# Kernel tuning notes

Hardware: AMD Instinct MI355X
Metric: run time of the kernel (lower is better)

## Reference

```python
import jax, jax.numpy as jnp
import numpy as np

B, S, D_IN, D_ST = 4, 4096, 1024, 1024


def setup_inputs() -> dict:
    key = jax.random.key(0)
    ks = jax.random.split(key, 7)
    s_in = 1.0 / np.sqrt(D_IN)
    s_st = 1.0 / np.sqrt(D_ST)
    return {
        "x": jax.random.normal(ks[0], (B, S, D_IN), dtype=jnp.float32),
        "gate_w": jax.random.uniform(ks[1], (D_IN, D_ST), jnp.float32, -s_in, s_in),
        "gate_b": jax.random.uniform(ks[2], (D_ST,), jnp.float32, -s_in, s_in),
        "inp_w": jax.random.uniform(ks[3], (D_IN, D_ST), jnp.float32, -s_in, s_in),
        "inp_b": jax.random.uniform(ks[4], (D_ST,), jnp.float32, -s_in, s_in),
        "out_w": jax.random.uniform(ks[5], (D_ST, D_IN), jnp.float32, -s_st, s_st),
        "out_b": jax.random.uniform(ks[6], (D_IN,), jnp.float32, -s_st, s_st),
    }


def reference(x, gate_w, gate_b, inp_w, inp_b, out_w, out_b):
    # x: [B, S, D_in]
    inp = jnp.einsum("bsd,de->bse", x, inp_w) + inp_b      # [B,S,Dst]
    gate = jax.nn.sigmoid(jnp.einsum("bsd,de->bse", x, gate_w) + gate_b)
    b_t = (1.0 - gate) * inp                               # [B,S,Dst]

    # affine recurrence h_t = gate_t * h_{t-1} + b_t via lax.scan over time
    def step(h, ab):
        a, b = ab
        h = a * h + b
        return h, h

    a_sb = jnp.swapaxes(gate, 0, 1)  # [S,B,Dst]
    b_sb = jnp.swapaxes(b_t, 0, 1)
    h0 = jnp.zeros((x.shape[0], inp.shape[-1]), dtype=x.dtype)
    _, hs = jax.lax.scan(step, h0, (a_sb, b_sb))           # [S,B,Dst]
    scan_out = jnp.swapaxes(hs, 0, 1)                      # [B,S,Dst]

    return x + jnp.einsum("bse,ed->bsd", scan_out, out_w) + out_b
```

## Files before the change

kernel.cpp:

```cpp
#include <hip/hip_runtime.h>

typedef unsigned short u16;
typedef unsigned int   u32;
typedef __bf16 bf16x8 __attribute__((ext_vector_type(8)));
typedef float  f32x4  __attribute__((ext_vector_type(4)));

#define DEVI __device__ __forceinline__

DEVI u16 f2bf(float f) {
    union { float f; u32 u; } c; c.f = f;
    u32 u = c.u;
    u32 r = (u + 0x7fffu + ((u >> 16) & 1u)) >> 16;
    return (u16)r;
}
DEVI float bf2f(u16 v) {
    union { u32 u; float f; } c; c.u = ((u32)v) << 16;
    return c.f;
}

DEVI void gload16(const void* g, void* l) {
    __builtin_amdgcn_global_load_lds(
        (const __attribute__((address_space(1))) void*)g,
        (__attribute__((address_space(3))) void*)l, 16, 0, 0);
}


#define VMW(N)  asm volatile("s_waitcnt vmcnt(" #N ")" ::: "memory")
#define BAR     __builtin_amdgcn_s_barrier()
#define SP1     __builtin_amdgcn_s_setprio(1)
#define SP0     __builtin_amdgcn_s_setprio(0)
#define SCB     __builtin_amdgcn_sched_barrier(0)
#define LGKM0   asm volatile("s_waitcnt lgkmcnt(0)" ::: "memory")
#define LGKM8   asm volatile("s_waitcnt lgkmcnt(8)" ::: "memory")

DEVI void stage_kh(const u16* g, u16* slot, int tid) {
    const int wvb = (tid >> 6) << 9;
    const int r = tid >> 2;
    const int p = tid & 3;
    const int c = p ^ (r & 3);
    const long off = (long)r * 1024 + (c << 3);
    gload16(g + off, slot + wvb);
    gload16(g + off + (long)128 * 1024, slot + 4096 + wvb);
}

DEVI f32x4 mfma(const bf16x8& a, const bf16x8& b, const f32x4& c) {
    return __builtin_amdgcn_mfma_f32_16x16x32_bf16(a, b, c, 0, 0, 0);
}

#define PHASE(I, Q, STAGE_CODE, GATE_CODE)                                   \
    {                                                                        \
        if (I == 0) {                                                        \
            _Pragma("unroll")                                                \
            for (int nf = 0; nf < 4; ++nf) {                                 \
                bh[nf][0] = *(const bf16x8*)(lds + (Q) + 16384 + nf * 512 + bbase); \
                bh[nf][1] = *(const bf16x8*)(lds + (Q) + 24576 + nf * 512 + bbase); \
            }                                                                \
        }                                                                    \
        a00 = *(const bf16x8*)(lds + (Q) + (I) * 1024 + abase);              \
        a01 = *(const bf16x8*)(lds + (Q) + 8192 + (I) * 1024 + abase);       \
        a10 = *(const bf16x8*)(lds + (Q) + (I) * 1024 + 512 + abase);        \
        a11 = *(const bf16x8*)(lds + (Q) + 8192 + (I) * 1024 + 512 + abase); \
        if (I == 0) { LGKM8; }                                               \
        STAGE_CODE;                                                          \
        SCB; BAR;                                                            \
        LGKM0; SCB;                                                          \
        SP1;                                                                 \
        _Pragma("unroll")                                                    \
        for (int nf = 0; nf < 4; ++nf) {                                     \
            acc[(I) * 2][nf]     = mfma(a00, bh[nf][0], acc[(I) * 2][nf]);   \
            acc[(I) * 2][nf]     = mfma(a01, bh[nf][1], acc[(I) * 2][nf]);   \
            acc[(I) * 2 + 1][nf] = mfma(a10, bh[nf][0], acc[(I) * 2 + 1][nf]); \
            acc[(I) * 2 + 1][nf] = mfma(a11, bh[nf][1], acc[(I) * 2 + 1][nf]); \
        }                                                                    \
        SP0;                                                                 \
        GATE_CODE;                                                           \
        BAR;                                                                 \
    }

#define NOSTAGE do {} while (0)
#define NOGATE  do {} while (0)

DEVI void pipe256(const u16* Ab, const u16* Bb, u16* lds,
                  f32x4 (&acc)[8][4], int tid) {
    const int lane = tid & 63;
    const int wm = (tid >> 6) >> 2, wn = (tid >> 6) & 3;
    const int pch = ((lane >> 4) ^ (lane & 3)) << 3;
    const int abase = (wm * 128 + (lane & 15)) * 32 + pch;
    const int bbase = (wn * 64 + (lane & 15)) * 32 + pch;

    stage_kh(Bb,      lds + 16384, tid);
    stage_kh(Bb + 32, lds + 24576, tid);
    stage_kh(Ab,      lds + 0,     tid);
    stage_kh(Ab + 32, lds + 8192,  tid);
    stage_kh(Bb + 64, lds + 49152, tid);
    stage_kh(Bb + 96, lds + 57344, tid);
    VMW(4); BAR;

    bf16x8 bh[4][2];
    bf16x8 a00, a01, a10, a11;

#pragma unroll 1
    for (int j = 0; j < 7; ++j) {
        const u16* A1g = Ab + (2 * j + 1) * 64;
        const u16* A2g = Ab + (2 * j + 2) * 64;
        const u16* B2g = Bb + (2 * j + 2) * 64;
        const u16* B3g = Bb + (2 * j + 3) * 64;
        PHASE(0, 0,
              { stage_kh(A1g, lds + 32768, tid); stage_kh(A1g + 32, lds + 40960, tid); },
              NOGATE);
        PHASE(1, 0,
              { stage_kh(B2g, lds + 16384, tid); stage_kh(B2g + 32, lds + 24576, tid); },
              NOGATE);
        PHASE(2, 0, NOSTAGE, NOGATE);
        PHASE(3, 0, NOSTAGE, VMW(4));
        PHASE(0, 32768,
              { stage_kh(A2g, lds + 0, tid); stage_kh(A2g + 32, lds + 8192, tid); },
              NOGATE);
        PHASE(1, 32768,
              { stage_kh(B3g, lds + 49152, tid); stage_kh(B3g + 32, lds + 57344, tid); },
              NOGATE);
        PHASE(2, 32768, NOSTAGE, NOGATE);
        PHASE(3, 32768, NOSTAGE, VMW(4));
    }
    {
        const u16* A15 = Ab + 15 * 64;
        PHASE(0, 0,
              { stage_kh(A15, lds + 32768, tid); stage_kh(A15 + 32, lds + 40960, tid); },
              NOGATE);
        PHASE(1, 0, NOSTAGE, NOGATE);
        PHASE(2, 0, NOSTAGE, NOGATE);
        PHASE(3, 0, NOSTAGE, VMW(0));
        PHASE(0, 32768, NOSTAGE, NOGATE);
        PHASE(1, 32768, NOSTAGE, NOGATE);
        PHASE(2, 32768, NOSTAGE, NOGATE);
        PHASE(3, 32768, NOSTAGE, NOGATE);
    }
}


__global__ __launch_bounds__(512, 1) void k_gemm_cat8(
    const u16* __restrict__ A, const u16* __restrict__ Bcat,
    const float* __restrict__ gb, const float* __restrict__ ib,
    u32* __restrict__ ab) {
    __shared__ __align__(16) u16 lds[65536];
    const int tid = threadIdx.x, lane = tid & 63;
    const int wm = (tid >> 6) >> 2, wn = (tid >> 6) & 3;

    int fid = (int)blockIdx.y * 8 + (int)blockIdx.x;
    int swz = (fid & 7) * 64 + (fid >> 3);
    const long bn = swz & 7, bm = swz >> 3;

    f32x4 acc[8][4] = {};
    pipe256(A + bm * 256 * 1024, Bcat + bn * 256 * 1024, lds, acc, tid);

    const long rbase = bm * 256 + wm * 128;
    const int chbase = (int)bn * 128 + wn * 32;
#pragma unroll
    for (int t = 0; t < 2; ++t) {
        int ch = chbase + t * 16 + (lane & 15);
        float g0 = gb[ch], i0 = ib[ch];
#pragma unroll
        for (int m = 0; m < 8; ++m) {
            long row = rbase + m * 16 + ((lane >> 4) << 2);
#pragma unroll
            for (int i = 0; i < 4; ++i) {
                float pg = acc[m][2 * t][i] + g0;
                float pi = acc[m][2 * t + 1][i] + i0;
                float aa = 1.0f / (1.0f + __expf(-pg));
                float bb = (1.0f - aa) * pi;
                ab[(row + i) * 1024 + ch] = (u32)f2bf(aa) | ((u32)f2bf(bb) << 16);
            }
        }
    }
}


__global__ __launch_bounds__(512, 1) void k_gemm_out8(
    const u16* __restrict__ A, const u16* __restrict__ Bt,
    const float* __restrict__ xres, const float* __restrict__ ob,
    float* __restrict__ out) {
    __shared__ __align__(16) u16 lds[65536];
    const int tid = threadIdx.x, lane = tid & 63;
    const int wm = (tid >> 6) >> 2, wn = (tid >> 6) & 3;

    int fid = (int)blockIdx.y * 4 + (int)blockIdx.x;
    int swz = (fid & 7) * 32 + (fid >> 3);
    const long bn = swz & 3, bm = swz >> 2;

    f32x4 acc[8][4] = {};
    pipe256(A + bm * 256 * 1024, Bt + bn * 256 * 1024, lds, acc, tid);

    const long rbase = bm * 256 + wm * 128;
    const int cbase = (int)bn * 256 + wn * 64;
#pragma unroll
    for (int n = 0; n < 4; ++n) {
        int col = cbase + n * 16 + (lane & 15);
        float o0 = ob[col];
#pragma unroll
        for (int m = 0; m < 8; ++m) {
            long row = rbase + m * 16 + ((lane >> 4) << 2);
#pragma unroll
            for (int i = 0; i < 4; ++i) {
                long o = (row + i) * 1024 + col;
                out[o] = acc[m][n][i] + o0 + xres[o];
            }
        }
    }
}


__global__ __launch_bounds__(256) void k_cvt_x(const float4* __restrict__ x,
                                               uint2* __restrict__ o, int n4) {
    int i = blockIdx.x * 256 + threadIdx.x;
    if (i < n4) {
        float4 v = x[i];
        uint2 r;
        r.x = (u32)f2bf(v.x) | ((u32)f2bf(v.y) << 16);
        r.y = (u32)f2bf(v.z) | ((u32)f2bf(v.w) << 16);
        o[i] = r;
    }
}

__global__ __launch_bounds__(256) void k_transpose_bf(const float* __restrict__ w,
                                                      u16* __restrict__ wt, int R, int C) {
    __shared__ float t[32][33];
    int c0 = blockIdx.x * 32, r0 = blockIdx.y * 32;
    int x = threadIdx.x & 31, y = threadIdx.x >> 5;
    for (int i = y; i < 32; i += 8) t[i][x] = w[(size_t)(r0 + i) * C + c0 + x];
    __syncthreads();
    for (int i = y; i < 32; i += 8) wt[(size_t)(c0 + i) * R + r0 + x] = f2bf(t[x][i]);
}

__global__ __launch_bounds__(256) void k_transpose_cat(const float* __restrict__ gw,
                                                       const float* __restrict__ iw,
                                                       u16* __restrict__ wt, int K, int C) {
    __shared__ float t[32][33];
    int c0 = blockIdx.x * 32, r0 = blockIdx.y * 32;
    const float* w = blockIdx.z ? iw : gw;
    int x = threadIdx.x & 31, y = threadIdx.x >> 5;
    for (int i = y; i < 32; i += 8) t[i][x] = w[(size_t)(r0 + i) * C + c0 + x];
    __syncthreads();
    for (int i = y; i < 32; i += 8) {
        int ch = c0 + i;
        int r = ((ch >> 4) << 5) | ((int)blockIdx.z << 4) | (ch & 15);
        wt[(size_t)r * K + r0 + x] = f2bf(t[x][i]);
    }
}


__global__ __launch_bounds__(256) void k_scanA(const u32* __restrict__ ab,
                                               float2* __restrict__ cAB) {
    int e = blockIdx.x * 256 + threadIdx.x;
    int c = blockIdx.y, bt = blockIdx.z;
    long base = ((long)bt * 4096 + c * 64) * 1024 + e;
    float Aa = 1.f, H = 0.f;
#pragma unroll 4
    for (int i = 0; i < 64; ++i) {
        u32 v = ab[base + (long)i * 1024];
        float a = bf2f((u16)v), b = bf2f((u16)(v >> 16));
        H = a * H + b;
        Aa *= a;
    }
    cAB[((long)bt * 64 + c) * 1024 + e] = make_float2(Aa, H);
}

__global__ __launch_bounds__(256) void k_scanB(const float2* __restrict__ cAB,
                                               float* __restrict__ hin) {
    int e = blockIdx.x * 256 + threadIdx.x;
    int bt = blockIdx.y;
    float H = 0.f;
#pragma unroll
    for (int c = 0; c < 64; ++c) {
        long s = ((long)bt * 64 + c) * 1024 + e;
        hin[s] = H;
        float2 v = cAB[s];
        H = v.x * H + v.y;
    }
}

__global__ __launch_bounds__(256) void k_scanC(const u32* __restrict__ ab,
                                               const float* __restrict__ hin,
                                               u16* __restrict__ hout) {
    int e = blockIdx.x * 256 + threadIdx.x;
    int c = blockIdx.y, bt = blockIdx.z;
    long base = ((long)bt * 4096 + c * 64) * 1024 + e;
    float H = hin[((long)bt * 64 + c) * 1024 + e];
#pragma unroll 4
    for (int i = 0; i < 64; ++i) {
        u32 v = ab[base + (long)i * 1024];
        H = bf2f((u16)v) * H + bf2f((u16)(v >> 16));
        hout[base + (long)i * 1024] = f2bf(H);
    }
}


extern "C" void kernel_launch(void* const* d_in, const int* in_sizes, int n_in,
                              void* d_out, int out_size, void* d_ws, size_t ws_size,
                              hipStream_t stream) {
    const float* x      = (const float*)d_in[0];
    const float* gate_w = (const float*)d_in[1];
    const float* gate_b = (const float*)d_in[2];
    const float* inp_w  = (const float*)d_in[3];
    const float* inp_b  = (const float*)d_in[4];
    const float* out_w  = (const float*)d_in[5];
    const float* out_b  = (const float*)d_in[6];
    float* out = (float*)d_out;

    const int Bsz = 4, S = 4096, Din = 1024, Dst = 1024;
    const int M = Bsz * S;
    const long nx = (long)M * Din;

    char* w = (char*)d_ws;
    u16* xb      = (u16*)(w);
    u16* catW    = (u16*)(w + 33554432);
    u16* owT     = (u16*)(w + 37748736);
    u16* hbf     = (u16*)(w + 39845888);
    float2* cAB  = (float2*)(w + 73400320);
    float* hin   = (float*)(w + 75497472);

    u32* ab = (u32*)d_out;

    k_cvt_x<<<(int)(nx / 4 / 256), 256, 0, stream>>>((const float4*)x, (uint2*)xb, (int)(nx / 4));
    k_transpose_cat<<<dim3(Dst / 32, Din / 32, 2), 256, 0, stream>>>(gate_w, inp_w, catW, Din, Dst);
    k_transpose_bf<<<dim3(Din / 32, Dst / 32), 256, 0, stream>>>(out_w, owT, Dst, Din);

    k_gemm_cat8<<<dim3(8, M / 256), 512, 0, stream>>>(xb, catW, gate_b, inp_b, ab);

    k_scanA<<<dim3(4, 64, Bsz), 256, 0, stream>>>(ab, cAB);
    k_scanB<<<dim3(4, Bsz), 256, 0, stream>>>(cAB, hin);
    k_scanC<<<dim3(4, 64, Bsz), 256, 0, stream>>>(ab, hin, hbf);

    k_gemm_out8<<<dim3(4, M / 256), 512, 0, stream>>>(hbf, owT, x, out_b, out);
}
```

Before: 187.5 us.

## Replace 64-K phased pipeline with triple-buffered 32-K tiles for two blocks per CU

The GEMM main loop moves from a double-buffered 64-wide K stage, with explicit lgkmcnt waits and sched barriers, to a rotating triple buffer of 32-wide K tiles with one barrier per tile. This shrinks LDS from 128KB to 96KB per block, and launch bounds change to allow two 512-thread blocks per CU, aiming for more occupancy and latency hiding. The risks are the added register pressure from the tighter launch bound, possible spills with an 8x4 accumulator array, and twice as many barriers per unit of K work.

```diff
diff --git a/kernel.cpp b/kernel.cpp
--- a/kernel.cpp
+++ b/kernel.cpp
@@ -29,9 +29,6 @@
 #define BAR     __builtin_amdgcn_s_barrier()
 #define SP1     __builtin_amdgcn_s_setprio(1)
 #define SP0     __builtin_amdgcn_s_setprio(0)
-#define SCB     __builtin_amdgcn_sched_barrier(0)
-#define LGKM0   asm volatile("s_waitcnt lgkmcnt(0)" ::: "memory")
-#define LGKM8   asm volatile("s_waitcnt lgkmcnt(8)" ::: "memory")
 
 DEVI void stage_kh(const u16* g, u16* slot, int tid) {
     const int wvb = (tid >> 6) << 9;
@@ -47,38 +44,48 @@
     return __builtin_amdgcn_mfma_f32_16x16x32_bf16(a, b, c, 0, 0, 0);
 }
 
-#define PHASE(I, Q, STAGE_CODE, GATE_CODE)                                   \
+#define TILE_COMPUTE(q0)                                                     \
     {                                                                        \
-        if (I == 0) {                                                        \
-            _Pragma("unroll")                                                \
-            for (int nf = 0; nf < 4; ++nf) {                                 \
-                bh[nf][0] = *(const bf16x8*)(lds + (Q) + 16384 + nf * 512 + bbase); \
-                bh[nf][1] = *(const bf16x8*)(lds + (Q) + 24576 + nf * 512 + bbase); \
-            }                                                                \
-        }                                                                    \
-        a00 = *(const bf16x8*)(lds + (Q) + (I) * 1024 + abase);              \
-        a01 = *(const bf16x8*)(lds + (Q) + 8192 + (I) * 1024 + abase);       \
-        a10 = *(const bf16x8*)(lds + (Q) + (I) * 1024 + 512 + abase);        \
-        a11 = *(const bf16x8*)(lds + (Q) + 8192 + (I) * 1024 + 512 + abase); \
-        if (I == 0) { LGKM8; }                                               \
-        STAGE_CODE;                                                          \
-        SCB; BAR;                                                            \
-        LGKM0; SCB;                                                          \
+        _Pragma("unroll")                                                    \
+        for (int nf = 0; nf < 4; ++nf)                                       \
+            bh[nf] = *(const bf16x8*)(lds + (q0) + bbase + nf * 512);        \
+        aC0 = *(const bf16x8*)(lds + (q0) + abase);                          \
+        aC1 = *(const bf16x8*)(lds + (q0) + abase + 512);                    \
+        aN0 = *(const bf16x8*)(lds + (q0) + abase + 1024);                   \
+        aN1 = *(const bf16x8*)(lds + (q0) + abase + 1536);                   \
         SP1;                                                                 \
         _Pragma("unroll")                                                    \
         for (int nf = 0; nf < 4; ++nf) {                                     \
-            acc[(I) * 2][nf]     = mfma(a00, bh[nf][0], acc[(I) * 2][nf]);   \
-            acc[(I) * 2][nf]     = mfma(a01, bh[nf][1], acc[(I) * 2][nf]);   \
-            acc[(I) * 2 + 1][nf] = mfma(a10, bh[nf][0], acc[(I) * 2 + 1][nf]); \
-            acc[(I) * 2 + 1][nf] = mfma(a11, bh[nf][1], acc[(I) * 2 + 1][nf]); \
+            acc[0][nf] = mfma(aC0, bh[nf], acc[0][nf]);                      \
+            acc[1][nf] = mfma(aC1, bh[nf], acc[1][nf]);                      \
         }                                                                    \
         SP0;                                                                 \
-        GATE_CODE;                                                           \
-        BAR;                                                                 \
-    }
-
-#define NOSTAGE do {} while (0)
-#define NOGATE  do {} while (0)
+        aC0 = *(const bf16x8*)(lds + (q0) + abase + 2048);                   \
+        aC1 = *(const bf16x8*)(lds + (q0) + abase + 2560);                   \
+        SP1;                                                                 \
+        _Pragma("unroll")                                                    \
+        for (int nf = 0; nf < 4; ++nf) {                                     \
+            acc[2][nf] = mfma(aN0, bh[nf], acc[2][nf]);                      \
+            acc[3][nf] = mfma(aN1, bh[nf], acc[3][nf]);                      \
+        }                                                                    \
+        SP0;                                                                 \
+        aN0 = *(const bf16x8*)(lds + (q0) + abase + 3072);                   \
+        aN1 = *(const bf16x8*)(lds + (q0) + abase + 3584);                   \
+        SP1;                                                                 \
+        _Pragma("unroll")                                                    \
+        for (int nf = 0; nf < 4; ++nf) {                                     \
+            acc[4][nf] = mfma(aC0, bh[nf], acc[4][nf]);                      \
+            acc[5][nf] = mfma(aC1, bh[nf], acc[5][nf]);                      \
+        }                                                                    \
+        SP0;                                                                 \
+        SP1;                                                                 \
+        _Pragma("unroll")                                                    \
+        for (int nf = 0; nf < 4; ++nf) {                                     \
+            acc[6][nf] = mfma(aN0, bh[nf], acc[6][nf]);                      \
+            acc[7][nf] = mfma(aN1, bh[nf], acc[7][nf]);                      \
+        }                                                                    \
+        SP0;                                                                 \
+    }
 
 DEVI void pipe256(const u16* Ab, const u16* Bb, u16* lds,
                   f32x4 (&acc)[8][4], int tid) {
@@ -86,63 +93,36 @@
     const int wm = (tid >> 6) >> 2, wn = (tid >> 6) & 3;
     const int pch = ((lane >> 4) ^ (lane & 3)) << 3;
     const int abase = (wm * 128 + (lane & 15)) * 32 + pch;
-    const int bbase = (wn * 64 + (lane & 15)) * 32 + pch;
-
-    stage_kh(Bb,      lds + 16384, tid);
+    const int bbase = 8192 + (wn * 64 + (lane & 15)) * 32 + pch;
+
+    stage_kh(Ab,      lds + 0,     tid);
+    stage_kh(Bb,      lds + 8192,  tid);
+    stage_kh(Ab + 32, lds + 16384, tid);
     stage_kh(Bb + 32, lds + 24576, tid);
-    stage_kh(Ab,      lds + 0,     tid);
-    stage_kh(Ab + 32, lds + 8192,  tid);
-    stage_kh(Bb + 64, lds + 49152, tid);
-    stage_kh(Bb + 96, lds + 57344, tid);
     VMW(4); BAR;
 
-    bf16x8 bh[4][2];
-    bf16x8 a00, a01, a10, a11;
+    bf16x8 bh[4], aC0, aC1, aN0, aN1;
+    int q0 = 0, q1 = 16384, q2 = 32768;
 
 #pragma unroll 1
-    for (int j = 0; j < 7; ++j) {
-        const u16* A1g = Ab + (2 * j + 1) * 64;
-        const u16* A2g = Ab + (2 * j + 2) * 64;
-        const u16* B2g = Bb + (2 * j + 2) * 64;
-        const u16* B3g = Bb + (2 * j + 3) * 64;
-        PHASE(0, 0,
-              { stage_kh(A1g, lds + 32768, tid); stage_kh(A1g + 32, lds + 40960, tid); },
-              NOGATE);
-        PHASE(1, 0,
-              { stage_kh(B2g, lds + 16384, tid); stage_kh(B2g + 32, lds + 24576, tid); },
-              NOGATE);
-        PHASE(2, 0, NOSTAGE, NOGATE);
-        PHASE(3, 0, NOSTAGE, VMW(4));
-        PHASE(0, 32768,
-              { stage_kh(A2g, lds + 0, tid); stage_kh(A2g + 32, lds + 8192, tid); },
-              NOGATE);
-        PHASE(1, 32768,
-              { stage_kh(B3g, lds + 49152, tid); stage_kh(B3g + 32, lds + 57344, tid); },
-              NOGATE);
-        PHASE(2, 32768, NOSTAGE, NOGATE);
-        PHASE(3, 32768, NOSTAGE, VMW(4));
-    }
-    {
-        const u16* A15 = Ab + 15 * 64;
-        PHASE(0, 0,
-              { stage_kh(A15, lds + 32768, tid); stage_kh(A15 + 32, lds + 40960, tid); },
-              NOGATE);
-        PHASE(1, 0, NOSTAGE, NOGATE);
-        PHASE(2, 0, NOSTAGE, NOGATE);
-        PHASE(3, 0, NOSTAGE, VMW(0));
-        PHASE(0, 32768, NOSTAGE, NOGATE);
-        PHASE(1, 32768, NOSTAGE, NOGATE);
-        PHASE(2, 32768, NOSTAGE, NOGATE);
-        PHASE(3, 32768, NOSTAGE, NOGATE);
-    }
-}
-
-
-__global__ __launch_bounds__(512, 1) void k_gemm_cat8(
+    for (int t = 0; t < 30; ++t) {
+        stage_kh(Ab + (t + 2) * 32, lds + q2, tid);
+        stage_kh(Bb + (t + 2) * 32, lds + q2 + 8192, tid);
+        TILE_COMPUTE(q0);
+        VMW(4); BAR;
+        int tq = q0; q0 = q1; q1 = q2; q2 = tq;
+    }
+    TILE_COMPUTE(q0);
+    VMW(0); BAR;
+    TILE_COMPUTE(q1);
+}
+
+
+__global__ __launch_bounds__(512, 2) void k_gemm_cat8(
     const u16* __restrict__ A, const u16* __restrict__ Bcat,
     const float* __restrict__ gb, const float* __restrict__ ib,
     u32* __restrict__ ab) {
-    __shared__ __align__(16) u16 lds[65536];
+    __shared__ __align__(16) u16 lds[49152];
     const int tid = threadIdx.x, lane = tid & 63;
     const int wm = (tid >> 6) >> 2, wn = (tid >> 6) & 3;
 
@@ -175,11 +155,11 @@
 }
 
 
-__global__ __launch_bounds__(512, 1) void k_gemm_out8(
+__global__ __launch_bounds__(512, 2) void k_gemm_out8(
     const u16* __restrict__ A, const u16* __restrict__ Bt,
     const float* __restrict__ xres, const float* __restrict__ ob,
     float* __restrict__ out) {
-    __shared__ __align__(16) u16 lds[65536];
+    __shared__ __align__(16) u16 lds[49152];
     const int tid = threadIdx.x, lane = tid & 63;
     const int wm = (tid >> 6) >> 2, wn = (tid >> 6) & 3;
 
```

Result: no change. 188.0 us (+0.2%).
